# Optimization experiments

Hardware: AMD Instinct MI355X
Metric: run time of the kernel (lower is better)

Reference implementation:

```python
import jax, jax.numpy as jnp
import numpy as np

B, C, H, W = 4, 256, 128, 128
K = 9  # 3x3 kernel taps


def _bilinear_gather(x, y, xq):
    """Bilinear sample x at float coords (y, xq) with zeros outside.
    x: [B,C,H,W]; y, xq: [B,K,H,W] -> returns [B,C,K,H,W]."""
    b, c, h, w = x.shape
    y0 = jnp.floor(y)
    x0 = jnp.floor(xq)
    wy = y - y0
    wx = xq - x0
    xf = x.reshape(b, c, h * w)

    def corner(yc, xc, wgt):
        valid = (yc >= 0) & (yc <= h - 1) & (xc >= 0) & (xc <= w - 1)
        yi = jnp.clip(yc, 0, h - 1).astype(jnp.int32)
        xi = jnp.clip(xc, 0, w - 1).astype(jnp.int32)
        idx = (yi * w + xi).reshape(b, -1)  # [B, K*H*W]
        g = jax.vmap(lambda xb, ib: jnp.take(xb, ib, axis=1))(xf, idx)
        g = g.reshape(b, c, *yc.shape[1:])  # [B,C,K,H,W]
        return g * (wgt * valid.astype(x.dtype))[:, None]

    v = corner(y0, x0, (1.0 - wy) * (1.0 - wx))
    v = v + corner(y0, x0 + 1.0, (1.0 - wy) * wx)
    v = v + corner(y0 + 1.0, x0, wy * (1.0 - wx))
    v = v + corner(y0 + 1.0, x0 + 1.0, wy * wx)
    return v


def setup_inputs() -> dict:
    key = jax.random.key(0)
    k1, k2, k3 = jax.random.split(key, 3)
    x = jax.random.normal(k1, (B, C, H, W), dtype=jnp.float32)
    offset = jax.random.normal(k2, (B, 2 * K, H, W), dtype=jnp.float32)
    weight = jax.random.normal(k3, (1, C, 3, 3), dtype=jnp.float32) / np.sqrt(C * K)
    bias = jnp.zeros((1,), dtype=jnp.float32)
    return {"x": x, "offset": offset, "weight": weight, "bias": bias}


def reference(x, offset, weight, bias):
    b, c, h, w = x.shape
    # offset channels ordered as (dy_k, dx_k) per kernel tap k (row-major 3x3)
    off = offset.reshape(b, K, 2, h, w)
    kyx = np.stack(np.meshgrid(np.arange(3), np.arange(3), indexing='ij'))  # [2,3,3]
    ky = jnp.asarray(kyx[0].reshape(K), x.dtype)
    kx = jnp.asarray(kyx[1].reshape(K), x.dtype)
    # sampling location: p0 (output pixel, stride 1, pad 1) + kernel tap + offset
    y = (jnp.arange(h, dtype=x.dtype)[None, None, :, None] - 1.0
         + ky[None, :, None, None] + off[:, :, 0])
    xq = (jnp.arange(w, dtype=x.dtype)[None, None, None, :] - 1.0
          + kx[None, :, None, None] + off[:, :, 1])
    sampled = _bilinear_gather(x, y, xq)  # [B,C,K,H,W]
    out = jnp.einsum('bckhw,ck->bhw', sampled, weight.reshape(c, K)) + bias
    return jax.nn.sigmoid(out)[:, None]  # [B,1,H,W]
```

## Files before the change

kernel.cpp:

```cpp
#include <hip/hip_runtime.h>
#include <math.h>

#define Bb 4
#define Cc 256
#define Hh 128
#define Ww 128
#define HW (Hh * Ww)
#define Kk 9

__global__ __launch_bounds__(256) void proj_kernel(const float* __restrict__ x,
                                                   const float* __restrict__ w,
                                                   float* __restrict__ D) {
    const int tid   = threadIdx.x;
    const int lane  = tid & 63;
    const int chunk = tid >> 6;
    const int bid   = blockIdx.x;
    const int b     = bid >> 8;
    const int pbase = (bid & 255) << 6;
    const int p     = pbase + lane;

    const int cu = __builtin_amdgcn_readfirstlane(chunk);
    const float* __restrict__ wp = w + cu * 64 * Kk;
    const float* __restrict__ xp = x + ((size_t)(b * Cc + cu * 64)) * HW + p;

    float acc[Kk];
#pragma unroll
    for (int k = 0; k < Kk; ++k) acc[k] = 0.f;

#pragma unroll 4
    for (int ci = 0; ci < 64; ++ci) {
        float xv = xp[(size_t)ci * HW];
#pragma unroll
        for (int k = 0; k < Kk; ++k) acc[k] += xv * wp[ci * Kk + k];
    }

    __shared__ float red[4][64][10];
#pragma unroll
    for (int k = 0; k < Kk; ++k) red[chunk][lane][k] = acc[k];
    __syncthreads();

    for (int idx = tid; idx < 64 * Kk; idx += 256) {
        const int k  = idx >> 6;
        const int px = idx & 63;
        float s = red[0][px][k] + red[1][px][k] + red[2][px][k] + red[3][px][k];
        D[((b * Kk + k) * HW) + pbase + px] = s;
    }
}

__global__ __launch_bounds__(256) void sample_kernel(const float* __restrict__ off,
                                                     const float* __restrict__ D,
                                                     const float* __restrict__ bias,
                                                     float* __restrict__ out) {
    const int g = blockIdx.x * 256 + threadIdx.x;
    const int b = g >> 14;
    const int p = g & (HW - 1);
    const int h = p >> 7;
    const int w = p & (Ww - 1);

    const float* __restrict__ offb = off + (size_t)b * (2 * Kk) * HW + p;
    const float* __restrict__ Db   = D + (size_t)b * Kk * HW;

    float s = bias[0];

#pragma unroll
    for (int k = 0; k < Kk; ++k) {
        const float dy = offb[(size_t)(2 * k) * HW];
        const float dx = offb[(size_t)(2 * k + 1) * HW];
        const float y  = (float)(h - 1 + (k / 3)) + dy;
        const float xq = (float)(w - 1 + (k % 3)) + dx;

        const float y0f = floorf(y);
        const float x0f = floorf(xq);
        const float wy  = y - y0f;
        const float wx  = xq - x0f;
        const int y0 = (int)y0f;
        const int x0 = (int)x0f;

        const float* __restrict__ Dk = Db + k * HW;

        {
            const int yy = y0, xx = x0;
            const bool valid = (yy >= 0) & (yy < Hh) & (xx >= 0) & (xx < Ww);
            const int yi = min(max(yy, 0), Hh - 1);
            const int xi = min(max(xx, 0), Ww - 1);
            const float v = Dk[yi * Ww + xi];
            s += valid ? (1.f - wy) * (1.f - wx) * v : 0.f;
        }
        {
            const int yy = y0, xx = x0 + 1;
            const bool valid = (yy >= 0) & (yy < Hh) & (xx >= 0) & (xx < Ww);
            const int yi = min(max(yy, 0), Hh - 1);
            const int xi = min(max(xx, 0), Ww - 1);
            const float v = Dk[yi * Ww + xi];
            s += valid ? (1.f - wy) * wx * v : 0.f;
        }
        {
            const int yy = y0 + 1, xx = x0;
            const bool valid = (yy >= 0) & (yy < Hh) & (xx >= 0) & (xx < Ww);
            const int yi = min(max(yy, 0), Hh - 1);
            const int xi = min(max(xx, 0), Ww - 1);
            const float v = Dk[yi * Ww + xi];
            s += valid ? wy * (1.f - wx) * v : 0.f;
        }
        {
            const int yy = y0 + 1, xx = x0 + 1;
            const bool valid = (yy >= 0) & (yy < Hh) & (xx >= 0) & (xx < Ww);
            const int yi = min(max(yy, 0), Hh - 1);
            const int xi = min(max(xx, 0), Ww - 1);
            const float v = Dk[yi * Ww + xi];
            s += valid ? wy * wx * v : 0.f;
        }
    }

    out[g] = 1.f / (1.f + expf(-s));
}

extern "C" void kernel_launch(void* const* d_in, const int* in_sizes, int n_in,
                              void* d_out, int out_size, void* d_ws, size_t ws_size,
                              hipStream_t stream) {
    const float* x    = (const float*)d_in[0];
    const float* off  = (const float*)d_in[1];
    const float* w    = (const float*)d_in[2];
    const float* bias = (const float*)d_in[3];
    float* out        = (float*)d_out;

    float* D = (float*)d_ws;

    proj_kernel<<<1024, 256, 0, stream>>>(x, w, D);
    sample_kernel<<<256, 256, 0, stream>>>(off, D, bias, out);
}
```

Before: 116.5 us.

## Vectorize projection loads and split sampling taps across waves

The projection kernel now has each lane handle four pixels with float4 loads across 8 channel chunks of 32. It uses 512-thread blocks with a two-stage shared-memory reduction. The sampling kernel splits the nine taps across three waves per 64 pixels and reduces them through shared memory, which raises the grid from 256 to 1024 blocks to improve occupancy on the latency-bound gather. The costs are fewer proj blocks (256), larger register use per thread, and extra synchronisation plus LDS traffic, including bank-conflict-prone strided writes with stride 9.

Result: faster. 110.7 us (-5.0%).

```diff
diff --git a/kernel.cpp b/kernel.cpp
--- a/kernel.cpp
+++ b/kernel.cpp
@@ -8,66 +8,89 @@
 #define HW (Hh * Ww)
 #define Kk 9
 
-__global__ __launch_bounds__(256) void proj_kernel(const float* __restrict__ x,
+__global__ __launch_bounds__(512) void proj_kernel(const float* __restrict__ x,
                                                    const float* __restrict__ w,
                                                    float* __restrict__ D) {
     const int tid   = threadIdx.x;
     const int lane  = tid & 63;
-    const int chunk = tid >> 6;
+    const int wv    = tid >> 6;
     const int bid   = blockIdx.x;
-    const int b     = bid >> 8;
-    const int pbase = (bid & 255) << 6;
-    const int p     = pbase + lane;
+    const int b     = bid >> 6;
+    const int pbase = (bid & 63) << 8;
+    const int p4    = pbase + lane * 4;
 
-    const int cu = __builtin_amdgcn_readfirstlane(chunk);
-    const float* __restrict__ wp = w + cu * 64 * Kk;
-    const float* __restrict__ xp = x + ((size_t)(b * Cc + cu * 64)) * HW + p;
+    const int cu = __builtin_amdgcn_readfirstlane(wv);
+    const float* __restrict__ wp = w + cu * 32 * Kk;
+    const float* __restrict__ xp = x + (size_t)(b * Cc + cu * 32) * HW + p4;
 
-    float acc[Kk];
+    float acc[Kk][4];
 #pragma unroll
-    for (int k = 0; k < Kk; ++k) acc[k] = 0.f;
+    for (int k = 0; k < Kk; ++k)
+#pragma unroll
+        for (int j = 0; j < 4; ++j) acc[k][j] = 0.f;
 
 #pragma unroll 4
-    for (int ci = 0; ci < 64; ++ci) {
-        float xv = xp[(size_t)ci * HW];
+    for (int ci = 0; ci < 32; ++ci) {
+        const float4 xv = *reinterpret_cast<const float4*>(xp + (size_t)ci * HW);
 #pragma unroll
-        for (int k = 0; k < Kk; ++k) acc[k] += xv * wp[ci * Kk + k];
+        for (int k = 0; k < Kk; ++k) {
+            const float wk = wp[ci * Kk + k];
+            acc[k][0] = fmaf(xv.x, wk, acc[k][0]);
+            acc[k][1] = fmaf(xv.y, wk, acc[k][1]);
+            acc[k][2] = fmaf(xv.z, wk, acc[k][2]);
+            acc[k][3] = fmaf(xv.w, wk, acc[k][3]);
+        }
     }
 
-    __shared__ float red[4][64][10];
+    __shared__ float red[4][256][Kk];
+    if (wv < 4) {
 #pragma unroll
-    for (int k = 0; k < Kk; ++k) red[chunk][lane][k] = acc[k];
+        for (int j = 0; j < 4; ++j)
+#pragma unroll
+            for (int k = 0; k < Kk; ++k) red[wv][lane * 4 + j][k] = acc[k][j];
+    }
+    __syncthreads();
+    if (wv >= 4) {
+#pragma unroll
+        for (int j = 0; j < 4; ++j)
+#pragma unroll
+            for (int k = 0; k < Kk; ++k) red[wv - 4][lane * 4 + j][k] += acc[k][j];
+    }
     __syncthreads();
 
-    for (int idx = tid; idx < 64 * Kk; idx += 256) {
-        const int k  = idx >> 6;
-        const int px = idx & 63;
-        float s = red[0][px][k] + red[1][px][k] + red[2][px][k] + red[3][px][k];
-        D[((b * Kk + k) * HW) + pbase + px] = s;
+    for (int idx = tid; idx < 256 * Kk; idx += 512) {
+        const int k  = idx >> 8;
+        const int px = idx & 255;
+        const float s = red[0][px][k] + red[1][px][k] + red[2][px][k] + red[3][px][k];
+        D[(b * Kk + k) * HW + pbase + px] = s;
     }
 }
 
-__global__ __launch_bounds__(256) void sample_kernel(const float* __restrict__ off,
+__global__ __launch_bounds__(192) void sample_kernel(const float* __restrict__ off,
                                                      const float* __restrict__ D,
                                                      const float* __restrict__ bias,
                                                      float* __restrict__ out) {
-    const int g = blockIdx.x * 256 + threadIdx.x;
-    const int b = g >> 14;
-    const int p = g & (HW - 1);
-    const int h = p >> 7;
-    const int w = p & (Ww - 1);
+    const int tid   = threadIdx.x;
+    const int lane  = tid & 63;
+    const int ktrio = tid >> 6;
+    const int bid   = blockIdx.x;
+    const int b     = bid >> 8;
+    const int p     = ((bid & 255) << 6) + lane;
+    const int h     = p >> 7;
+    const int w_    = p & (Ww - 1);
 
     const float* __restrict__ offb = off + (size_t)b * (2 * Kk) * HW + p;
     const float* __restrict__ Db   = D + (size_t)b * Kk * HW;
 
-    float s = bias[0];
+    float s = 0.f;
 
 #pragma unroll
-    for (int k = 0; k < Kk; ++k) {
+    for (int j = 0; j < 3; ++j) {
+        const int k = ktrio * 3 + j;
         const float dy = offb[(size_t)(2 * k) * HW];
         const float dx = offb[(size_t)(2 * k + 1) * HW];
-        const float y  = (float)(h - 1 + (k / 3)) + dy;
-        const float xq = (float)(w - 1 + (k % 3)) + dx;
+        const float y  = (float)(h - 1 + ktrio) + dy;
+        const float xq = (float)(w_ - 1 + j) + dx;
 
         const float y0f = floorf(y);
         const float x0f = floorf(xq);
@@ -112,7 +135,14 @@
         }
     }
 
-    out[g] = 1.f / (1.f + expf(-s));
+    __shared__ float part[3][64];
+    part[ktrio][lane] = s;
+    __syncthreads();
+
+    if (tid < 64) {
+        const float t = part[0][lane] + part[1][lane] + part[2][lane] + bias[0];
+        out[(b << 14) + ((bid & 255) << 6) + lane] = 1.f / (1.f + expf(-t));
+    }
 }
 
 extern "C" void kernel_launch(void* const* d_in, const int* in_sizes, int n_in,
@@ -126,6 +156,6 @@
 
     float* D = (float*)d_ws;
 
-    proj_kernel<<<1024, 256, 0, stream>>>(x, w, D);
-    sample_kernel<<<256, 256, 0, stream>>>(off, D, bias, out);
+    proj_kernel<<<256, 512, 0, stream>>>(x, w, D);
+    sample_kernel<<<1024, 192, 0, stream>>>(off, D, bias, out);
 }
```
